# Performance work log

Hardware: AMD Instinct MI355X
Metric: run time of the kernel (lower is better)

## Reference

```python
import jax, jax.numpy as jnp
import numpy as np

HIDDEN = 256


def setup_inputs() -> dict:
    key = jax.random.key(0)
    k1, k2, k3, k4, k5 = jax.random.split(key, 5)
    B, N, T, I, H = 64, 16, 128, 256, HIDDEN
    return {
        "x": jax.random.normal(k1, (B, N, T, I), dtype=jnp.float32),
        "weight_ih": jax.random.normal(k2, (1, N, 3 * H, I), dtype=jnp.float32) * 0.05,
        "weight_hh": jax.random.normal(k3, (1, N, 3 * H, H), dtype=jnp.float32) * 0.05,
        "bias_ih": jax.random.normal(k4, (1, N, 3 * H), dtype=jnp.float32) * 0.05,
        "bias_hh": jax.random.normal(k5, (1, N, 3 * H), dtype=jnp.float32) * 0.05,
    }


def _gru_scan(x, weight_ih, weight_hh, bias_ih, bias_hh):
    H = HIDDEN
    wih = weight_ih[0]  # [N, 3H, I]
    whh = weight_hh[0]  # [N, 3H, H]
    bih = bias_ih       # [1, N, 3H] broadcasts over batch
    bhh = bias_hh
    xt = jnp.transpose(x, (2, 0, 1, 3))  # [T, B, N, I]
    B, N = xt.shape[1], xt.shape[2]
    h0 = jnp.zeros((B, N, H), dtype=x.dtype)

    def step(h, x_t):
        ih = jnp.einsum('bni,ngi->bng', x_t, wih) + bih   # [B, N, 3H]
        hh = jnp.einsum('bnh,ngh->bng', h, whh) + bhh     # [B, N, 3H]
        rz = jax.nn.sigmoid(ih[..., :2 * H] + hh[..., :2 * H])
        r, z = rz[..., :H], rz[..., H:]
        n = jnp.tanh(ih[..., 2 * H:] + r * hh[..., 2 * H:])
        h_new = (1 - z) * n + z * h
        return h_new, h_new

    _, ys = jax.lax.scan(step, h0, xt)      # ys: [T, B, N, H]
    return jnp.transpose(ys, (1, 2, 0, 3))  # [B, N, T, H] (batch_first, output_num=-1)


def reference(x, weight_ih, weight_hh, bias_ih, bias_hh):
    return _gru_scan(x, weight_ih, weight_hh, bias_ih, bias_hh)
```

## Files before the change

### kernel.cpp

```cpp
#include <hip/hip_runtime.h>
#include <stdint.h>

#define B_ 64
#define N_ 16
#define T_ 128
#define I_ 256
#define H_ 256
#define G_ 768
#define TC 64

typedef __attribute__((ext_vector_type(8))) short bf8;
typedef __attribute__((ext_vector_type(8))) unsigned short u16x8;
typedef __attribute__((ext_vector_type(4))) float f4;

static __device__ __forceinline__ unsigned short f2bf(float f) {
    uint32_t u = __builtin_bit_cast(uint32_t, f);
    u += 0x7fffu + ((u >> 16) & 1u);
    return (unsigned short)(u >> 16);
}
static __device__ __forceinline__ float bf2f(unsigned short s) {
    return __builtin_bit_cast(float, ((uint32_t)s) << 16);
}
static __device__ __forceinline__ float sigm(float x) {
    return __builtin_amdgcn_rcpf(1.f + __expf(-x));
}

#define OFF_WIH   0ull
#define OFF_WHH   6291456ull
#define OFF_BIAS  12582912ull
#define OFF_H32   12632064ull
#define OFF_IH    13680640ull
#define WS_NEEDED (OFF_IH + 100663296ull)

__global__ __launch_bounds__(256) void prep_kernel(
        const float* __restrict__ wih, const float* __restrict__ whh,
        const float* __restrict__ bih, const float* __restrict__ bhh,
        unsigned char* ws) {
    unsigned short* wih_bf = (unsigned short*)(ws + OFF_WIH);
    unsigned short* whh_fr = (unsigned short*)(ws + OFF_WHH);
    float* bias_f = (float*)(ws + OFF_BIAS);
    int gid = blockIdx.x * blockDim.x + threadIdx.x;
    int nthr = gridDim.x * blockDim.x;

    for (int o = gid; o < 393216; o += nthr) {
        const float* s = wih + (size_t)o * 8;
        u16x8 v;
        #pragma unroll
        for (int e = 0; e < 8; e++) v[e] = f2bf(s[e]);
        *(u16x8*)(wih_bf + (size_t)o * 8) = v;
    }
    for (int o = gid; o < 393216; o += nthr) {
        int lane = o & 63, kt = (o >> 6) & 7, ct = (o >> 9) % 48, n = o / 24576;
        int gcol = ct * 16 + (lane & 15);
        int k0 = kt * 32 + (lane >> 4) * 8;
        const float* s = whh + ((size_t)(n * G_ + gcol)) * H_ + k0;
        u16x8 v;
        #pragma unroll
        for (int e = 0; e < 8; e++) v[e] = f2bf(s[e]);
        *(u16x8*)(whh_fr + (size_t)o * 8) = v;
    }
    for (int o = gid; o < N_ * G_; o += nthr) {
        int g = o % G_;
        bias_f[o] = bih[o] + (g < 512 ? bhh[o] : 0.f);
    }
}

__global__ __launch_bounds__(512, 2) void ih_gemm(
        const float* __restrict__ x, const unsigned char* __restrict__ wsr,
        unsigned char* ws, int t0) {
    const unsigned short* wih_bf = (const unsigned short*)(wsr + OFF_WIH);
    const float* bias_f = (const float*)(wsr + OFF_BIAS);
    unsigned short* IH = (unsigned short*)(ws + OFF_IH);

    __shared__ __align__(16) unsigned short As[64 * 256];
    __shared__ __align__(16) unsigned short Bs[128 * 256];

    int tid = threadIdx.x;
    int lane = tid & 63, w = tid >> 6;
    int wr = w >> 2, wc = w & 3;
    int n = blockIdx.x >> 6, b = blockIdx.x & 63;

    {
        const float* xb = x + (((size_t)(b * N_ + n)) * T_ + t0) * I_;
        #pragma unroll
        for (int i = 0; i < 4; i++) {
            int chunk = i * 512 + tid;
            int row = chunk >> 5, c16 = chunk & 31;
            const float* s = xb + row * I_ + c16 * 8;
            float4 f0 = *(const float4*)s;
            float4 f1 = *(const float4*)(s + 4);
            u16x8 v;
            v[0] = f2bf(f0.x); v[1] = f2bf(f0.y); v[2] = f2bf(f0.z); v[3] = f2bf(f0.w);
            v[4] = f2bf(f1.x); v[5] = f2bf(f1.y); v[6] = f2bf(f1.z); v[7] = f2bf(f1.w);
            int eoff = row * 256 + ((c16 * 8) ^ ((row & 7) << 3));
            *(u16x8*)(As + eoff) = v;
        }
    }

    for (int ct = 0; ct < 6; ct++) {
        #pragma unroll
        for (int i = 0; i < 8; i++) {
            int chunk = i * 512 + tid;
            int row = chunk >> 5, c16 = chunk & 31;
            u16x8 v = *(const u16x8*)(wih_bf + ((size_t)(n * G_ + ct * 128 + row)) * I_ + c16 * 8);
            int eoff = row * 256 + ((c16 * 8) ^ ((row & 7) << 3));
            *(u16x8*)(Bs + eoff) = v;
        }
        __syncthreads();

        f4 acc[2][2];
        f4 zf = {0.f, 0.f, 0.f, 0.f};
        #pragma unroll
        for (int m = 0; m < 2; m++)
            #pragma unroll
            for (int nb2 = 0; nb2 < 2; nb2++) acc[m][nb2] = zf;

        int q16 = (lane >> 4) * 8;
        #pragma unroll
        for (int kt = 0; kt < 8; kt++) {
            bf8 a[2], bb[2];
            #pragma unroll
            for (int m = 0; m < 2; m++) {
                int ar = wr * 32 + m * 16 + (lane & 15);
                a[m] = *(const bf8*)(As + ar * 256 + ((kt * 32 + q16) ^ ((ar & 7) << 3)));
            }
            #pragma unroll
            for (int nb2 = 0; nb2 < 2; nb2++) {
                int br = wc * 32 + nb2 * 16 + (lane & 15);
                bb[nb2] = *(const bf8*)(Bs + br * 256 + ((kt * 32 + q16) ^ ((br & 7) << 3)));
            }
            #pragma unroll
            for (int m = 0; m < 2; m++)
                #pragma unroll
                for (int nb2 = 0; nb2 < 2; nb2++)
                    acc[m][nb2] = __builtin_amdgcn_mfma_f32_16x16x32_bf16(a[m], bb[nb2], acc[m][nb2], 0, 0, 0);
        }

        #pragma unroll
        for (int nb2 = 0; nb2 < 2; nb2++) {
            int col = wc * 32 + nb2 * 16 + (lane & 15);
            int g = ct * 128 + col;
            float bias = bias_f[n * G_ + g];
            #pragma unroll
            for (int m = 0; m < 2; m++) {
                #pragma unroll
                for (int r = 0; r < 4; r++) {
                    int trow = wr * 32 + m * 16 + (lane >> 4) * 4 + r;
                    size_t oidx = ((size_t)(b * N_ + n) * TC + trow) * G_ + g;
                    IH[oidx] = f2bf(acc[m][nb2][r] + bias);
                }
            }
        }
        __syncthreads();
    }
}

__global__ __launch_bounds__(512, 2) void gru_scan(
        const unsigned char* __restrict__ wsr, unsigned char* ws,
        const float* __restrict__ bhh, float* __restrict__ out,
        int chunk, int t0) {
    const unsigned short* IH = (const unsigned short*)(wsr + OFF_IH);
    const unsigned short* whh_fr = (const unsigned short*)(wsr + OFF_WHH);
    float* h32ws = (float*)(ws + OFF_H32);

    __shared__ __align__(16) unsigned short hbf[2][4][272];

    int tid = threadIdx.x, lane = tid & 63, w = tid >> 6;
    int n = blockIdx.x & 15, rg = blockIdx.x >> 4;

    int c16 = lane & 15;
    int q = lane >> 4;
    int hrow = c16 >> 2;
    int q16 = q * 8;
    int brow = rg * 4 + q;

    bf8 wf[3][2][8];
    #pragma unroll
    for (int g = 0; g < 3; g++)
        #pragma unroll
        for (int u = 0; u < 2; u++) {
            int ct = g * 16 + w * 2 + u;
            #pragma unroll
            for (int kt = 0; kt < 8; kt++)
                wf[g][u][kt] = *(const bf8*)(whh_fr + ((((size_t)n * 48 + ct) * 8 + kt) * 64 + lane) * 8);
        }

    int colb = w * 32 + c16;
    float bn0 = bhh[n * G_ + 512 + colb];
    float bn1 = bhh[n * G_ + 512 + colb + 16];
    float h0 = 0.f, h1 = 0.f;
    if (chunk) {
        const float* hp = h32ws + ((size_t)brow * N_ + n) * H_ + colb;
        h0 = hp[0]; h1 = hp[16];
    }
    hbf[0][q][colb] = f2bf(h0);
    hbf[0][q][colb + 16] = f2bf(h1);

    const unsigned short* ihp = IH + ((size_t)(brow * N_ + n) * TC) * G_ + colb;

    unsigned short c_r0 = ihp[0],   c_r1 = ihp[16];
    unsigned short c_z0 = ihp[256], c_z1 = ihp[272];
    unsigned short c_n0 = ihp[512], c_n1 = ihp[528];
    ihp += G_;

    f4 zf = {0.f, 0.f, 0.f, 0.f};
    __syncthreads();

    #pragma unroll 1
    for (int t = 0; t < TC; t++) {
        const unsigned short* pp = (t + 1 < TC) ? ihp : (ihp - G_);
        unsigned short n_r0 = pp[0],   n_r1 = pp[16];
        unsigned short n_z0 = pp[256], n_z1 = pp[272];
        unsigned short n_n0 = pp[512], n_n1 = pp[528];
        ihp += G_;

        const unsigned short* hb = &hbf[t & 1][0][0];
        f4 acc[3][2];
        #pragma unroll
        for (int g = 0; g < 3; g++)
            #pragma unroll
            for (int u = 0; u < 2; u++) acc[g][u] = zf;
        #pragma unroll
        for (int kt = 0; kt < 8; kt++) {
            bf8 a = *(const bf8*)(hb + hrow * 272 + kt * 32 + q16);
            #pragma unroll
            for (int g = 0; g < 3; g++)
                #pragma unroll
                for (int u = 0; u < 2; u++)
                    acc[g][u] = __builtin_amdgcn_mfma_f32_16x16x32_bf16(a, wf[g][u][kt], acc[g][u], 0, 0, 0);
        }

        float xr0 = bf2f(c_r0) + acc[0][0][0];
        float xz0 = bf2f(c_z0) + acc[1][0][0];
        float rr0 = sigm(xr0), zz0 = sigm(xz0);
        float pre0 = bf2f(c_n0) + rr0 * (acc[2][0][0] + bn0);
        float e20 = __expf(2.f * pre0);
        float nv0 = 1.f - 2.f * __builtin_amdgcn_rcpf(e20 + 1.f);
        float hn0 = nv0 + zz0 * (h0 - nv0);

        float xr1 = bf2f(c_r1) + acc[0][1][0];
        float xz1 = bf2f(c_z1) + acc[1][1][0];
        float rr1 = sigm(xr1), zz1 = sigm(xz1);
        float pre1 = bf2f(c_n1) + rr1 * (acc[2][1][0] + bn1);
        float e21 = __expf(2.f * pre1);
        float nv1 = 1.f - 2.f * __builtin_amdgcn_rcpf(e21 + 1.f);
        float hn1 = nv1 + zz1 * (h1 - nv1);

        h0 = hn0; h1 = hn1;

        unsigned short* hw = &hbf[(t & 1) ^ 1][q][colb];
        hw[0] = f2bf(hn0);
        hw[16] = f2bf(hn1);

        float* op = out + ((size_t)(brow * N_ + n) * T_ + (t0 + t)) * H_ + colb;
        op[0] = hn0;
        op[16] = hn1;

        c_r0 = n_r0; c_r1 = n_r1;
        c_z0 = n_z0; c_z1 = n_z1;
        c_n0 = n_n0; c_n1 = n_n1;

        __syncthreads();
    }

    float* hp = h32ws + ((size_t)brow * N_ + n) * H_ + colb;
    hp[0] = h0;
    hp[16] = h1;
}

extern "C" void kernel_launch(void* const* d_in, const int* in_sizes, int n_in,
                              void* d_out, int out_size, void* d_ws, size_t ws_size,
                              hipStream_t stream) {
    const float* x   = (const float*)d_in[0];
    const float* wih = (const float*)d_in[1];
    const float* whh = (const float*)d_in[2];
    const float* bih = (const float*)d_in[3];
    const float* bhh = (const float*)d_in[4];
    float* out = (float*)d_out;
    unsigned char* ws = (unsigned char*)d_ws;

    if (ws_size < WS_NEEDED) return;

    prep_kernel<<<1024, 256, 0, stream>>>(wih, whh, bih, bhh, ws);
    for (int chunk = 0; chunk < 2; chunk++) {
        int t0 = chunk * TC;
        ih_gemm<<<dim3(1024), 512, 0, stream>>>(x, ws, ws, t0);
        gru_scan<<<dim3(256), 512, 0, stream>>>(ws, ws, bhh, out, chunk, t0);
    }
}
```

Before: 325.6 us.

## Pre-swizzle W_ih into MFMA fragment layout and stream B from global

The prep kernel now writes W_ih in the same per-lane MFMA fragment order already used for W_hh. The ih_gemm kernel then drops its shared-memory B tile and the per-column-tile loop with its barriers. Each wave instead owns 6 column tiles across all 64 rows and loads B fragments straight from global memory, prefetching the next k-step into registers. This removes the LDS staging and synchronisation for B, at the cost of many more accumulator registers (24 f4 tiles per wave), which may lower occupancy.

```diff
diff --git a/kernel.cpp b/kernel.cpp
--- a/kernel.cpp
+++ b/kernel.cpp
@@ -36,28 +36,23 @@
         const float* __restrict__ wih, const float* __restrict__ whh,
         const float* __restrict__ bih, const float* __restrict__ bhh,
         unsigned char* ws) {
-    unsigned short* wih_bf = (unsigned short*)(ws + OFF_WIH);
+    unsigned short* wih_fr = (unsigned short*)(ws + OFF_WIH);
     unsigned short* whh_fr = (unsigned short*)(ws + OFF_WHH);
     float* bias_f = (float*)(ws + OFF_BIAS);
     int gid = blockIdx.x * blockDim.x + threadIdx.x;
     int nthr = gridDim.x * blockDim.x;
 
     for (int o = gid; o < 393216; o += nthr) {
-        const float* s = wih + (size_t)o * 8;
-        u16x8 v;
-        #pragma unroll
-        for (int e = 0; e < 8; e++) v[e] = f2bf(s[e]);
-        *(u16x8*)(wih_bf + (size_t)o * 8) = v;
-    }
-    for (int o = gid; o < 393216; o += nthr) {
         int lane = o & 63, kt = (o >> 6) & 7, ct = (o >> 9) % 48, n = o / 24576;
         int gcol = ct * 16 + (lane & 15);
         int k0 = kt * 32 + (lane >> 4) * 8;
-        const float* s = whh + ((size_t)(n * G_ + gcol)) * H_ + k0;
-        u16x8 v;
-        #pragma unroll
-        for (int e = 0; e < 8; e++) v[e] = f2bf(s[e]);
-        *(u16x8*)(whh_fr + (size_t)o * 8) = v;
+        const float* s0 = wih + ((size_t)(n * G_ + gcol)) * I_ + k0;
+        const float* s1 = whh + ((size_t)(n * G_ + gcol)) * H_ + k0;
+        u16x8 v0, v1;
+        #pragma unroll
+        for (int e = 0; e < 8; e++) { v0[e] = f2bf(s0[e]); v1[e] = f2bf(s1[e]); }
+        *(u16x8*)(wih_fr + (size_t)o * 8) = v0;
+        *(u16x8*)(whh_fr + (size_t)o * 8) = v1;
     }
     for (int o = gid; o < N_ * G_; o += nthr) {
         int g = o % G_;
@@ -68,90 +63,82 @@
 __global__ __launch_bounds__(512, 2) void ih_gemm(
         const float* __restrict__ x, const unsigned char* __restrict__ wsr,
         unsigned char* ws, int t0) {
-    const unsigned short* wih_bf = (const unsigned short*)(wsr + OFF_WIH);
+    const unsigned short* wih_fr = (const unsigned short*)(wsr + OFF_WIH);
     const float* bias_f = (const float*)(wsr + OFF_BIAS);
     unsigned short* IH = (unsigned short*)(ws + OFF_IH);
 
     __shared__ __align__(16) unsigned short As[64 * 256];
-    __shared__ __align__(16) unsigned short Bs[128 * 256];
-
-    int tid = threadIdx.x;
-    int lane = tid & 63, w = tid >> 6;
-    int wr = w >> 2, wc = w & 3;
+
+    int tid = threadIdx.x, lane = tid & 63, w = tid >> 6;
     int n = blockIdx.x >> 6, b = blockIdx.x & 63;
+    int c16 = lane & 15, q = lane >> 4, q16 = q * 8;
 
     {
         const float* xb = x + (((size_t)(b * N_ + n)) * T_ + t0) * I_;
         #pragma unroll
         for (int i = 0; i < 4; i++) {
             int chunk = i * 512 + tid;
-            int row = chunk >> 5, c16 = chunk & 31;
-            const float* s = xb + row * I_ + c16 * 8;
+            int row = chunk >> 5, kc = chunk & 31;
+            const float* s = xb + row * I_ + kc * 8;
             float4 f0 = *(const float4*)s;
             float4 f1 = *(const float4*)(s + 4);
             u16x8 v;
             v[0] = f2bf(f0.x); v[1] = f2bf(f0.y); v[2] = f2bf(f0.z); v[3] = f2bf(f0.w);
             v[4] = f2bf(f1.x); v[5] = f2bf(f1.y); v[6] = f2bf(f1.z); v[7] = f2bf(f1.w);
-            int eoff = row * 256 + ((c16 * 8) ^ ((row & 7) << 3));
+            int eoff = row * 256 + ((kc * 8) ^ ((row & 7) << 3));
             *(u16x8*)(As + eoff) = v;
         }
     }
-
-    for (int ct = 0; ct < 6; ct++) {
-        #pragma unroll
-        for (int i = 0; i < 8; i++) {
-            int chunk = i * 512 + tid;
-            int row = chunk >> 5, c16 = chunk & 31;
-            u16x8 v = *(const u16x8*)(wih_bf + ((size_t)(n * G_ + ct * 128 + row)) * I_ + c16 * 8);
-            int eoff = row * 256 + ((c16 * 8) ^ ((row & 7) << 3));
-            *(u16x8*)(Bs + eoff) = v;
-        }
-        __syncthreads();
-
-        f4 acc[2][2];
-        f4 zf = {0.f, 0.f, 0.f, 0.f};
-        #pragma unroll
-        for (int m = 0; m < 2; m++)
-            #pragma unroll
-            for (int nb2 = 0; nb2 < 2; nb2++) acc[m][nb2] = zf;
-
-        int q16 = (lane >> 4) * 8;
-        #pragma unroll
-        for (int kt = 0; kt < 8; kt++) {
-            bf8 a[2], bb[2];
-            #pragma unroll
-            for (int m = 0; m < 2; m++) {
-                int ar = wr * 32 + m * 16 + (lane & 15);
-                a[m] = *(const bf8*)(As + ar * 256 + ((kt * 32 + q16) ^ ((ar & 7) << 3)));
+    __syncthreads();
+
+    const unsigned short* bptr = wih_fr + (((size_t)n * 48 + w * 6) * 8) * 64 * 8;
+
+    f4 acc[4][6];
+    f4 zf = {0.f, 0.f, 0.f, 0.f};
+    #pragma unroll
+    for (int rt = 0; rt < 4; rt++)
+        #pragma unroll
+        for (int c = 0; c < 6; c++) acc[rt][c] = zf;
+
+    bf8 bc[6], bn[6];
+    #pragma unroll
+    for (int c = 0; c < 6; c++)
+        bc[c] = *(const bf8*)(bptr + (((size_t)c * 8 + 0) * 64 + lane) * 8);
+
+    #pragma unroll 1
+    for (int kt = 0; kt < 8; kt++) {
+        int ktn = (kt + 1) & 7;
+        #pragma unroll
+        for (int c = 0; c < 6; c++)
+            bn[c] = *(const bf8*)(bptr + (((size_t)c * 8 + ktn) * 64 + lane) * 8);
+        bf8 a[4];
+        #pragma unroll
+        for (int rt = 0; rt < 4; rt++) {
+            int ar = rt * 16 + c16;
+            a[rt] = *(const bf8*)(As + ar * 256 + ((kt * 32 + q16) ^ ((ar & 7) << 3)));
+        }
+        #pragma unroll
+        for (int c = 0; c < 6; c++)
+            #pragma unroll
+            for (int rt = 0; rt < 4; rt++)
+                acc[rt][c] = __builtin_amdgcn_mfma_f32_16x16x32_bf16(a[rt], bc[c], acc[rt][c], 0, 0, 0);
+        #pragma unroll
+        for (int c = 0; c < 6; c++) bc[c] = bn[c];
+    }
+
+    size_t obase = (size_t)(b * N_ + n) * TC;
+    #pragma unroll
+    for (int c = 0; c < 6; c++) {
+        int g = (w * 6 + c) * 16 + c16;
+        float bias = bias_f[n * G_ + g];
+        #pragma unroll
+        for (int rt = 0; rt < 4; rt++) {
+            #pragma unroll
+            for (int r = 0; r < 4; r++) {
+                int trow = rt * 16 + q * 4 + r;
+                IH[(obase + trow) * G_ + g] = f2bf(acc[rt][c][r] + bias);
             }
-            #pragma unroll
-            for (int nb2 = 0; nb2 < 2; nb2++) {
-                int br = wc * 32 + nb2 * 16 + (lane & 15);
-                bb[nb2] = *(const bf8*)(Bs + br * 256 + ((kt * 32 + q16) ^ ((br & 7) << 3)));
-            }
-            #pragma unroll
-            for (int m = 0; m < 2; m++)
-                #pragma unroll
-                for (int nb2 = 0; nb2 < 2; nb2++)
-                    acc[m][nb2] = __builtin_amdgcn_mfma_f32_16x16x32_bf16(a[m], bb[nb2], acc[m][nb2], 0, 0, 0);
-        }
-
-        #pragma unroll
-        for (int nb2 = 0; nb2 < 2; nb2++) {
-            int col = wc * 32 + nb2 * 16 + (lane & 15);
-            int g = ct * 128 + col;
-            float bias = bias_f[n * G_ + g];
-            #pragma unroll
-            for (int m = 0; m < 2; m++) {
-                #pragma unroll
-                for (int r = 0; r < 4; r++) {
-                    int trow = wr * 32 + m * 16 + (lane >> 4) * 4 + r;
-                    size_t oidx = ((size_t)(b * N_ + n) * TC + trow) * G_ + g;
-                    IH[oidx] = f2bf(acc[m][nb2][r] + bias);
-                }
-            }
-        }
-        __syncthreads();
+        }
     }
 }
 
```

Measured after the change: 314.1 us. -3.5%, faster.
